# Kernel tuning notes

Measured on AMD Instinct MI355X. Metric: run time of the kernel, lower is better.

Reference implementation:

```python
import jax, jax.numpy as jnp
import numpy as np

G, N, F_IN, D, R, E, L = 512, 128, 64, 128, 4, 1572864, 2  # graphs, nodes/graph, in-feat, embed, relations, edges, gnn layers


def setup_inputs() -> dict:
    key = jax.random.key(0)
    ks = jax.random.split(key, 8)
    x = jax.random.normal(ks[0], (G * N, F_IN), jnp.float32)
    # edges are within-graph (disjoint batched graph, as built by batch_to_gd)
    gid = jax.random.randint(ks[1], (E,), 0, G)
    loc = jax.random.randint(ks[2], (2, E), 0, N)
    edge_index = gid[None, :] * N + loc  # [2, E] (src, dst)
    edge_attr = jax.random.randint(ks[3], (E,), 0, R)
    W_emb = jax.random.normal(ks[4], (F_IN, D), jnp.float32) / np.sqrt(F_IN)
    b_emb = jnp.zeros((D,), jnp.float32)
    W_root = jax.random.normal(ks[5], (L, D, D), jnp.float32) / np.sqrt(D)
    W_rel = jax.random.normal(ks[6], (L, R, D, D), jnp.float32) / np.sqrt(D)
    bias = jnp.zeros((L, D), jnp.float32)
    return {"x": x, "edge_index": edge_index, "edge_attr": edge_attr,
            "W_emb": W_emb, "b_emb": b_emb, "W_root": W_root, "W_rel": W_rel, "bias": bias}


def rgcn_layer(h, edge_index, edge_attr, W_root_l, W_rel_l, bias_l):
    # PyG RGCNConv: out_i = h_i @ W_root + sum_r mean_{j in N_r(i)} (h_j @ W_r) + bias
    n = h.shape[0]
    xr = jnp.einsum('nd,rde->rne', h, W_rel_l)          # [R, n, D] per-relation transform
    src, dst = edge_index[0], edge_index[1]
    msg = xr[edge_attr, src]                             # [E, D] gather per edge
    seg = dst * R + edge_attr                            # combined (node, relation) segment id
    summed = jax.ops.segment_sum(msg, seg, num_segments=n * R)
    cnt = jax.ops.segment_sum(jnp.ones((msg.shape[0],), h.dtype), seg, num_segments=n * R)
    mean = summed / jnp.maximum(cnt, 1.0)[:, None]       # per-relation mean aggregation
    agg = mean.reshape(n, R, -1).sum(axis=1)             # sum over relations
    return h @ W_root_l + agg + bias_l


def reference(x, edge_index, edge_attr, W_emb, b_emb, W_root, W_rel, bias):
    h = x @ W_emb + b_emb                                # embedding_linear
    for l in range(L):                                   # mp_rounds = 1 per layer
        h = jax.nn.relu(rgcn_layer(h, edge_index, edge_attr, W_root[l], W_rel[l], bias[l]))
    # split into per-graph chunks of N nodes and max-pool over nodes
    return jnp.max(h.reshape(G, N, -1), axis=1)          # [G, D]
```

## Files before the change

kernel.cpp:

```cpp
#include <hip/hip_runtime.h>

constexpr int GG    = 512;
constexpr int NPG   = 128;
constexpr int FIN   = 64;
constexpr int DD    = 128;
constexpr int RR    = 4;
constexpr int NN    = GG * NPG;
constexpr int EE    = 1572864;
constexpr int SLC   = 4096;
constexpr int HSTR  = 136;

typedef __attribute__((ext_vector_type(8))) _Float16 f16x8;
typedef __attribute__((ext_vector_type(2))) _Float16 f16x2;
typedef __attribute__((ext_vector_type(4))) float f32x4;
typedef unsigned short u16;
typedef unsigned int   u32;

__device__ __forceinline__ u16 f16b(float x) {
    _Float16 h = (_Float16)x;
    return __builtin_bit_cast(u16, h);
}
__device__ __forceinline__ f16x2 as2(u32 w) { return __builtin_bit_cast(f16x2, w); }

__device__ __forceinline__ void gl_lds16(const void* g, void* l) {
    __builtin_amdgcn_global_load_lds((const __attribute__((address_space(1))) u32*)g,
                                     (__attribute__((address_space(3))) u32*)l, 16, 0, 0);
}


__global__ __launch_bounds__(256, 2) void k_front(const int* __restrict__ ei,
                                                  const int* __restrict__ ea,
                                                  u32* __restrict__ bcur,
                                                  u16* __restrict__ binned,
                                                  const float* __restrict__ W_root,
                                                  const float* __restrict__ W_rel,
                                                  const float* __restrict__ W_emb,
                                                  u16* __restrict__ wtH) {
    __shared__ u32 sRec[4096];
    __shared__ int bh[512];
    __shared__ int lcur[512];
    __shared__ float tile[32 * 129];
    int tid = threadIdx.x;
    int bid = blockIdx.x;

    if (bid < 384) {
        int e0 = bid * 4096;
        bh[tid] = 0; bh[tid + 256] = 0;
        __syncthreads();
        for (int i = 0; i < 16; ++i) {
            int e = e0 + i * 256 + tid;
            int src = ei[e];
            int dst = ei[EE + e];
            int a   = ea[e];
            int g   = dst >> 7;
            u32 rec = (u32)(src & 127) | ((u32)(dst & 127) << 7) | ((u32)a << 14);
            sRec[i * 256 + tid] = rec | ((u32)g << 16);
            atomicAdd(&bh[g], 1);
        }
        __syncthreads();
        lcur[tid]       = tid * SLC +
                          (int)atomicAdd(&bcur[tid], (u32)bh[tid]);
        lcur[tid + 256] = (tid + 256) * SLC +
                          (int)atomicAdd(&bcur[tid + 256], (u32)bh[tid + 256]);
        __syncthreads();
        for (int i = 0; i < 16; ++i) {
            u32 r = sRec[i * 256 + tid];
            int pos = atomicAdd(&lcur[r >> 16], 1);
            binned[pos] = (u16)(r & 0xFFFFu);
        }
    } else if (bid < 424) {
        int pb = bid - 384;
        int mat = pb >> 2;
        int k0 = (pb & 3) * 32;
        int l = mat / 5, m5 = mat - l * 5;
        const float* Wsrc = (m5 == 0) ? (W_root + l * 16384)
                                      : (W_rel + (size_t)(l * RR + (m5 - 1)) * 16384);
        for (int i = 0; i < 16; ++i) {
            int k = k0 + (tid >> 7) + i * 2;
            int n = tid & 127;
            tile[(k - k0) * 129 + n] = Wsrc[k * 128 + n];
        }
        __syncthreads();
        for (int i = 0; i < 16; ++i) {
            int kk = tid & 31;
            int n  = (tid >> 5) + i * 8;
            wtH[mat * 16384 + n * 128 + k0 + kk] = f16b(tile[kk * 129 + n]);
        }
    } else {
        int k0 = (bid - 424) * 32;
        for (int i = 0; i < 16; ++i) {
            int k = k0 + (tid >> 7) + i * 2;
            int n = tid & 127;
            tile[(k - k0) * 129 + n] = W_emb[k * 128 + n];
        }
        __syncthreads();
        for (int i = 0; i < 16; ++i) {
            int kk = tid & 31;
            int n  = (tid >> 5) + i * 8;
            wtH[163840 + n * 64 + k0 + kk] = f16b(tile[kk * 129 + n]);
        }
    }
}


__global__ __launch_bounds__(512, 4) void k_fused(const float* __restrict__ x,
                                                  const float* __restrict__ b_emb,
                                                  float* __restrict__ outF,
                                                  const u16* __restrict__ wtH,
                                                  const float* __restrict__ bias,
                                                  const u16* __restrict__ binned,
                                                  const u32* __restrict__ bcur) {
    __shared__ __align__(16) u16 hG[128 * HSTR];
    __shared__ __align__(16) u16 sQ[2][8192];
    __shared__ __align__(16) u16 sIdx[SLC];
    __shared__ int   sOffs[512];
    __shared__ int   sCnt[512];
    __shared__ float sInv[512];

    int tid  = threadIdx.x;
    int wave = tid >> 6, lane = tid & 63;
    int mm   = lane & 15;
    int qd   = lane >> 4;
    int gr   = blockIdx.x;
    int row0g = gr * NPG;
    int strip = wave * 16;
    const u16* wtE = wtH + 163840;

    auto stage = [&](int step, int bufi) {
        const u16* src = wtH + (step >> 1) * 16384 + (step & 1) * 64;
#pragma unroll
        for (int i = 0; i < 2; ++i) {
            int u = i * 512 + tid;
            int n = u >> 3, j = u & 7;
            gl_lds16(src + n * 128 + ((j ^ (n & 7)) * 8), &sQ[bufi][u * 8]);
        }
    };
    auto stageE = [&](int bufi) {
#pragma unroll
        for (int i = 0; i < 2; ++i) {
            int u = i * 512 + tid;
            int n = u >> 3, j = u & 7;
            gl_lds16(wtE + n * 64 + ((j ^ (n & 7)) * 8), &sQ[bufi][u * 8]);
        }
    };

    f32x4 acc[8];
    auto mfma_half = [&](int bufi, f16x8 A0, f16x8 A1) {
        const u16* buf = sQ[bufi];
#pragma unroll
        for (int nt = 0; nt < 8; ++nt) {
            int n = nt * 16 + mm;
            int g0 = n * 8 + ((0 * 4 + qd) ^ (n & 7));
            int g1 = n * 8 + ((1 * 4 + qd) ^ (n & 7));
            f16x8 B0 = *(const f16x8*)&buf[g0 * 8];
            f16x8 B1 = *(const f16x8*)&buf[g1 * 8];
            f32x4 a = acc[nt];
            a = __builtin_amdgcn_mfma_f32_16x16x32_f16(A0, B0, a, 0, 0, 0);
            a = __builtin_amdgcn_mfma_f32_16x16x32_f16(A1, B1, a, 0, 0, 0);
            acc[nt] = a;
        }
    };

    auto gather = [&](int rel, f16x8* AH) {
        int key = (rel << 7) + strip + mm;
        int r0 = sOffs[key];
        int r1 = sCnt[key];
        _Float16 hs = (_Float16)sInv[key];
        f16x2 sv; sv[0] = hs; sv[1] = hs;
        int cb = qd * 8;
        f16x2 ax[16];
#pragma unroll
        for (int i = 0; i < 16; ++i) ax[i] = (f16x2){(_Float16)0.f, (_Float16)0.f};
        auto add8 = [&](int ks, uint4 u) {
            ax[ks * 4 + 0] += as2(u.x);
            ax[ks * 4 + 1] += as2(u.y);
            ax[ks * 4 + 2] += as2(u.z);
            ax[ks * 4 + 3] += as2(u.w);
        };
        int j = r0;
        for (; j + 2 <= r1; j += 2) {
            int rb0 = (int)sIdx[j]     * HSTR + cb;
            int rb1 = (int)sIdx[j + 1] * HSTR + cb;
            uint4 a0 = *(const uint4*)&hG[rb0];
            uint4 a1 = *(const uint4*)&hG[rb0 + 32];
            uint4 a2 = *(const uint4*)&hG[rb0 + 64];
            uint4 a3 = *(const uint4*)&hG[rb0 + 96];
            uint4 b0 = *(const uint4*)&hG[rb1];
            uint4 b1 = *(const uint4*)&hG[rb1 + 32];
            uint4 b2 = *(const uint4*)&hG[rb1 + 64];
            uint4 b3 = *(const uint4*)&hG[rb1 + 96];
            add8(0, a0); add8(1, a1); add8(2, a2); add8(3, a3);
            add8(0, b0); add8(1, b1); add8(2, b2); add8(3, b3);
        }
        if (j < r1) {
            int rb = (int)sIdx[j] * HSTR + cb;
            uint4 a0 = *(const uint4*)&hG[rb];
            uint4 a1 = *(const uint4*)&hG[rb + 32];
            uint4 a2 = *(const uint4*)&hG[rb + 64];
            uint4 a3 = *(const uint4*)&hG[rb + 96];
            add8(0, a0); add8(1, a1); add8(2, a2); add8(3, a3);
        }
#pragma unroll
        for (int q = 0; q < 4; ++q) {
            union { u32 w[4]; f16x8 v; } o;
#pragma unroll
            for (int t = 0; t < 4; ++t) {
                f16x2 r = ax[q * 4 + t] * sv;
                o.w[t] = __builtin_bit_cast(u32, r);
            }
            AH[q] = o.v;
        }
    };

    stageE(0);
    int cnt = (int)bcur[gr];
    if (cnt > SLC) cnt = SLC;
    uint4 myRec = *(const uint4*)&binned[gr * SLC + tid * 8];
    sCnt[tid] = 0;
    __syncthreads();
    int base8 = tid * 8;
#pragma unroll
    for (int i = 0; i < 8; ++i) {
        if (base8 + i < cnt) {
            u32 w = ((const u32*)&myRec)[i >> 1];
            u32 rec = (i & 1) ? (w >> 16) : (w & 0xFFFFu);
            atomicAdd(&sCnt[rec >> 7], 1);
        }
    }
    __syncthreads();
    int c = sCnt[tid];
    int v = c;
#pragma unroll
    for (int o = 1; o < 64; o <<= 1) {
        int t = __shfl_up(v, o);
        if (lane >= o) v += t;
    }
    int* wtot = (int*)sIdx;
    if (lane == 63) wtot[wave] = v;
    __syncthreads();
    int base = 0;
#pragma unroll
    for (int w = 0; w < 8; ++w) {
        int tw = wtot[w];
        if (w < wave) base += tw;
    }
    int ex = base + v - c;
    sOffs[tid] = ex;
    sCnt[tid]  = ex;
    sInv[tid]  = 1.0f / (float)(c > 0 ? c : 1);
    __syncthreads();
#pragma unroll
    for (int i = 0; i < 8; ++i) {
        if (base8 + i < cnt) {
            u32 w = ((const u32*)&myRec)[i >> 1];
            u32 rec = (i & 1) ? (w >> 16) : (w & 0xFFFFu);
            int pos = atomicAdd(&sCnt[rec >> 7], 1);
            sIdx[pos] = (u16)(rec & 127u);
        }
    }
    __syncthreads();

    {
#pragma unroll
        for (int nt = 0; nt < 8; ++nt) {
            float bv = b_emb[nt * 16 + mm];
            acc[nt] = (f32x4){bv, bv, bv, bv};
        }
        f16x8 AE[2];
#pragma unroll
        for (int ks = 0; ks < 2; ++ks) {
            const float* xp = &x[(size_t)(row0g + strip + mm) * FIN + ks * 32 + qd * 8];
            float4 a = *(const float4*)xp;
            float4 b = *(const float4*)(xp + 4);
            union { u32 w[4]; f16x8 v; } o;
            o.w[0] = (u32)f16b(a.x) | ((u32)f16b(a.y) << 16);
            o.w[1] = (u32)f16b(a.z) | ((u32)f16b(a.w) << 16);
            o.w[2] = (u32)f16b(b.x) | ((u32)f16b(b.y) << 16);
            o.w[3] = (u32)f16b(b.z) | ((u32)f16b(b.w) << 16);
            AE[ks] = o.v;
        }
        stage(0, 1);
        mfma_half(0, AE[0], AE[1]);
#pragma unroll
        for (int nt = 0; nt < 8; ++nt)
#pragma unroll
            for (int r = 0; r < 4; ++r)
                hG[(strip + qd * 4 + r) * HSTR + nt * 16 + mm] =
                    f16b(acc[nt][r]);
        __syncthreads();
    }

    for (int L = 0; L < 2; ++L) {
        const float* bl = bias + L * DD;
#pragma unroll
        for (int i = 0; i < 8; ++i) acc[i] = (f32x4){0.f, 0.f, 0.f, 0.f};

        f16x8 AH[4];
#pragma unroll
        for (int ks = 0; ks < 4; ++ks)
            AH[ks] = *(const f16x8*)&hG[(strip + mm) * HSTR + ks * 32 + qd * 8];

        for (int m = 0; m < 5; ++m) {
#pragma unroll
            for (int h = 0; h < 2; ++h) {
                int s = L * 10 + m * 2 + h;
                if (s + 1 < 20) stage(s + 1, s & 1);
                mfma_half((s + 1) & 1, AH[h * 2], AH[h * 2 + 1]);
                __syncthreads();
            }
            if (m < 4) gather(m, AH);
        }

        if (L == 0) {
#pragma unroll
            for (int nt = 0; nt < 8; ++nt) {
                float bv = bl[nt * 16 + mm];
#pragma unroll
                for (int r = 0; r < 4; ++r)
                    hG[(strip + qd * 4 + r) * HSTR + nt * 16 + mm] =
                        f16b(fmaxf(acc[nt][r] + bv, 0.f));
            }
            __syncthreads();
        } else {
            float* red = (float*)sIdx;
#pragma unroll
            for (int nt = 0; nt < 8; ++nt) {
                float bv = bl[nt * 16 + mm];
                float vv = fmaxf(fmaxf(acc[nt][0], acc[nt][1]),
                                 fmaxf(acc[nt][2], acc[nt][3])) + bv;
                vv = fmaxf(vv, 0.f);
                vv = fmaxf(vv, __shfl_xor(vv, 16));
                vv = fmaxf(vv, __shfl_xor(vv, 32));
                if (lane < 16) red[wave * 128 + nt * 16 + mm] = vv;
            }
            __syncthreads();
            if (tid < 128) {
                float mx = red[tid];
#pragma unroll
                for (int w = 1; w < 8; ++w) mx = fmaxf(mx, red[w * 128 + tid]);
                outF[gr * DD + tid] = mx;
            }
        }
    }
}


extern "C" void kernel_launch(void* const* d_in, const int* in_sizes, int n_in,
                              void* d_out, int out_size, void* d_ws, size_t ws_size,
                              hipStream_t stream) {
    const float* x      = (const float*)d_in[0];
    const int*   ei     = (const int*)  d_in[1];
    const int*   ea     = (const int*)  d_in[2];
    const float* W_emb  = (const float*)d_in[3];
    const float* b_emb  = (const float*)d_in[4];
    const float* W_root = (const float*)d_in[5];
    const float* W_rel  = (const float*)d_in[6];
    const float* bias   = (const float*)d_in[7];
    float* out = (float*)d_out;

    char* p = (char*)d_ws;
    u32* bcur   = (u32*)p; p += 2048;
    u16* binned = (u16*)p; p += (size_t)GG * SLC * 2;
    u16* wtH    = (u16*)p; p += (size_t)(10 * 16384 + 8192) * 2;

    (void)hipMemsetAsync(bcur, 0, 2048, stream);

    k_front<<<426, 256, 0, stream>>>(ei, ea, bcur, binned,
                                     W_root, W_rel, W_emb, wtH);
    k_fused<<<GG, 512, 0, stream>>>(x, b_emb, out, wtH, bias, binned, bcur);
}
```

Before: 164.0 us.

## Locally sort edge records in LDS before binning and pad global bin counters

The binning blocks now do a block-wide prefix scan over per-graph counts, scatter records into a sorted LDS buffer, then write them to global memory in sorted order, so consecutive threads write contiguous runs within each graph's slice instead of scattered 2-byte stores. The global per-graph atomic counters are spread 32 words apart to avoid contention on the same cache line. This adds a scan, extra LDS passes and barriers, and a larger memset.

```diff
diff --git a/kernel.cpp b/kernel.cpp
--- a/kernel.cpp
+++ b/kernel.cpp
@@ -9,6 +9,7 @@
 constexpr int EE    = 1572864;
 constexpr int SLC   = 4096;
 constexpr int HSTR  = 136;
+constexpr int BPAD  = 32;
 
 typedef __attribute__((ext_vector_type(8))) _Float16 f16x8;
 typedef __attribute__((ext_vector_type(2))) _Float16 f16x2;
@@ -39,6 +40,9 @@
     __shared__ u32 sRec[4096];
     __shared__ int bh[512];
     __shared__ int lcur[512];
+    __shared__ int lstart[512];
+    __shared__ int gbase[512];
+    __shared__ int wt4[4];
     __shared__ float tile[32 * 129];
     int tid = threadIdx.x;
     int bid = blockIdx.x;
@@ -58,15 +62,43 @@
             atomicAdd(&bh[g], 1);
         }
         __syncthreads();
-        lcur[tid]       = tid * SLC +
-                          (int)atomicAdd(&bcur[tid], (u32)bh[tid]);
-        lcur[tid + 256] = (tid + 256) * SLC +
-                          (int)atomicAdd(&bcur[tid + 256], (u32)bh[tid + 256]);
-        __syncthreads();
+        int c0 = bh[2 * tid], c1 = bh[2 * tid + 1];
+        int s  = c0 + c1;
+        int v  = s;
+        int lane = tid & 63, wv = tid >> 6;
+#pragma unroll
+        for (int o = 1; o < 64; o <<= 1) {
+            int t = __shfl_up(v, o);
+            if (lane >= o) v += t;
+        }
+        if (lane == 63) wt4[wv] = v;
+        gbase[2 * tid]     = (2 * tid) * SLC +
+                             (int)atomicAdd(&bcur[(2 * tid) * BPAD], (u32)c0);
+        gbase[2 * tid + 1] = (2 * tid + 1) * SLC +
+                             (int)atomicAdd(&bcur[(2 * tid + 1) * BPAD], (u32)c1);
+        __syncthreads();
+        int base = 0;
+#pragma unroll
+        for (int w = 0; w < 4; ++w)
+            if (w < wv) base += wt4[w];
+        int ex = base + v - s;
+        lstart[2 * tid]     = ex;
+        lstart[2 * tid + 1] = ex + c0;
+        lcur[2 * tid]       = ex;
+        lcur[2 * tid + 1]   = ex + c0;
+        __syncthreads();
+        u32* sorted = (u32*)tile;
         for (int i = 0; i < 16; ++i) {
             u32 r = sRec[i * 256 + tid];
             int pos = atomicAdd(&lcur[r >> 16], 1);
-            binned[pos] = (u16)(r & 0xFFFFu);
+            sorted[pos] = r;
+        }
+        __syncthreads();
+        for (int i = 0; i < 16; ++i) {
+            int p = i * 256 + tid;
+            u32 r = sorted[p];
+            int g = r >> 16;
+            binned[gbase[g] + (p - lstart[g])] = (u16)(r & 0xFFFFu);
         }
     } else if (bid < 424) {
         int pb = bid - 384;
@@ -213,7 +245,7 @@
     };
 
     stageE(0);
-    int cnt = (int)bcur[gr];
+    int cnt = (int)bcur[gr * BPAD];
     if (cnt > SLC) cnt = SLC;
     uint4 myRec = *(const uint4*)&binned[gr * SLC + tid * 8];
     sCnt[tid] = 0;
@@ -359,11 +391,11 @@
     float* out = (float*)d_out;
 
     char* p = (char*)d_ws;
-    u32* bcur   = (u32*)p; p += 2048;
+    u32* bcur   = (u32*)p; p += (size_t)512 * BPAD * 4;
     u16* binned = (u16*)p; p += (size_t)GG * SLC * 2;
     u16* wtH    = (u16*)p; p += (size_t)(10 * 16384 + 8192) * 2;
 
-    (void)hipMemsetAsync(bcur, 0, 2048, stream);
+    (void)hipMemsetAsync(bcur, 0, (size_t)512 * BPAD * 4, stream);
 
     k_front<<<426, 256, 0, stream>>>(ei, ea, bcur, binned,
                                      W_root, W_rel, W_emb, wtH);
```

After: 162.2 us. Within noise of the previous version (-1.1%).

## Merge edge binning and weight conversion into fused kernel with grid barrier

Applied to the files above, without the earlier changes.

Folds the separate front kernel (edge binning by graph and weight transpose/fp16 conversion) into the main fused kernel, joined by a software grid-wide barrier on an atomic counter. It removes one kernel launch and its gap. The binning is also reworked: each block sorts its edges locally in LDS and then writes contiguous runs per graph. Per-graph counters are padded to separate cache lines to reduce atomic contention. The cost is that the grid barrier assumes all 512 blocks are co-resident; if they are not, the kernel deadlocks.

```diff
diff --git a/kernel.cpp b/kernel.cpp
--- a/kernel.cpp
+++ b/kernel.cpp
@@ -9,6 +9,8 @@
 constexpr int EE    = 1572864;
 constexpr int SLC   = 4096;
 constexpr int HSTR  = 136;
+constexpr int BPAD  = 32;
+constexpr int WTN   = 10 * 16384 + 8192;
 
 typedef __attribute__((ext_vector_type(8))) _Float16 f16x8;
 typedef __attribute__((ext_vector_type(2))) _Float16 f16x2;
@@ -28,88 +30,19 @@
 }
 
 
-__global__ __launch_bounds__(256, 2) void k_front(const int* __restrict__ ei,
-                                                  const int* __restrict__ ea,
-                                                  u32* __restrict__ bcur,
-                                                  u16* __restrict__ binned,
-                                                  const float* __restrict__ W_root,
-                                                  const float* __restrict__ W_rel,
-                                                  const float* __restrict__ W_emb,
-                                                  u16* __restrict__ wtH) {
-    __shared__ u32 sRec[4096];
-    __shared__ int bh[512];
-    __shared__ int lcur[512];
-    __shared__ float tile[32 * 129];
-    int tid = threadIdx.x;
-    int bid = blockIdx.x;
-
-    if (bid < 384) {
-        int e0 = bid * 4096;
-        bh[tid] = 0; bh[tid + 256] = 0;
-        __syncthreads();
-        for (int i = 0; i < 16; ++i) {
-            int e = e0 + i * 256 + tid;
-            int src = ei[e];
-            int dst = ei[EE + e];
-            int a   = ea[e];
-            int g   = dst >> 7;
-            u32 rec = (u32)(src & 127) | ((u32)(dst & 127) << 7) | ((u32)a << 14);
-            sRec[i * 256 + tid] = rec | ((u32)g << 16);
-            atomicAdd(&bh[g], 1);
-        }
-        __syncthreads();
-        lcur[tid]       = tid * SLC +
-                          (int)atomicAdd(&bcur[tid], (u32)bh[tid]);
-        lcur[tid + 256] = (tid + 256) * SLC +
-                          (int)atomicAdd(&bcur[tid + 256], (u32)bh[tid + 256]);
-        __syncthreads();
-        for (int i = 0; i < 16; ++i) {
-            u32 r = sRec[i * 256 + tid];
-            int pos = atomicAdd(&lcur[r >> 16], 1);
-            binned[pos] = (u16)(r & 0xFFFFu);
-        }
-    } else if (bid < 424) {
-        int pb = bid - 384;
-        int mat = pb >> 2;
-        int k0 = (pb & 3) * 32;
-        int l = mat / 5, m5 = mat - l * 5;
-        const float* Wsrc = (m5 == 0) ? (W_root + l * 16384)
-                                      : (W_rel + (size_t)(l * RR + (m5 - 1)) * 16384);
-        for (int i = 0; i < 16; ++i) {
-            int k = k0 + (tid >> 7) + i * 2;
-            int n = tid & 127;
-            tile[(k - k0) * 129 + n] = Wsrc[k * 128 + n];
-        }
-        __syncthreads();
-        for (int i = 0; i < 16; ++i) {
-            int kk = tid & 31;
-            int n  = (tid >> 5) + i * 8;
-            wtH[mat * 16384 + n * 128 + k0 + kk] = f16b(tile[kk * 129 + n]);
-        }
-    } else {
-        int k0 = (bid - 424) * 32;
-        for (int i = 0; i < 16; ++i) {
-            int k = k0 + (tid >> 7) + i * 2;
-            int n = tid & 127;
-            tile[(k - k0) * 129 + n] = W_emb[k * 128 + n];
-        }
-        __syncthreads();
-        for (int i = 0; i < 16; ++i) {
-            int kk = tid & 31;
-            int n  = (tid >> 5) + i * 8;
-            wtH[163840 + n * 64 + k0 + kk] = f16b(tile[kk * 129 + n]);
-        }
-    }
-}
-
-
 __global__ __launch_bounds__(512, 4) void k_fused(const float* __restrict__ x,
                                                   const float* __restrict__ b_emb,
                                                   float* __restrict__ outF,
-                                                  const u16* __restrict__ wtH,
+                                                  u16* __restrict__ wtH,
                                                   const float* __restrict__ bias,
-                                                  const u16* __restrict__ binned,
-                                                  const u32* __restrict__ bcur) {
+                                                  u16* __restrict__ binned,
+                                                  u32* __restrict__ bcur,
+                                                  u32* __restrict__ gctr,
+                                                  const int* __restrict__ ei,
+                                                  const int* __restrict__ ea,
+                                                  const float* __restrict__ W_root,
+                                                  const float* __restrict__ W_rel,
+                                                  const float* __restrict__ W_emb) {
     __shared__ __align__(16) u16 hG[128 * HSTR];
     __shared__ __align__(16) u16 sQ[2][8192];
     __shared__ __align__(16) u16 sIdx[SLC];
@@ -125,6 +58,90 @@
     int row0g = gr * NPG;
     int strip = wave * 16;
     const u16* wtE = wtH + 163840;
+
+    {
+        int idx = gr * 512 + tid;
+        if (idx < WTN) {
+            float s;
+            if (idx < 163840) {
+                int mat = idx >> 14, rem = idx & 16383;
+                int n = rem >> 7, k = rem & 127;
+                int l = mat / 5, m5 = mat - l * 5;
+                const float* Wsrc = (m5 == 0) ? (W_root + l * 16384)
+                                              : (W_rel + (size_t)(l * RR + (m5 - 1)) * 16384);
+                s = Wsrc[k * 128 + n];
+            } else {
+                int d2 = idx - 163840;
+                int n = d2 >> 6, k = d2 & 63;
+                s = W_emb[k * 128 + n];
+            }
+            wtH[idx] = f16b(s);
+        }
+
+        u32* sRec   = (u32*)&sQ[0][0];
+        u32* sorted = sRec + 3072;
+        int* gbaseA = (int*)(sRec + 6144);
+        int* wt8    = (int*)sIdx;
+        int e0 = gr * 3072;
+        sCnt[tid] = 0;
+        __syncthreads();
+#pragma unroll
+        for (int i = 0; i < 6; ++i) {
+            int e = e0 + i * 512 + tid;
+            int src = ei[e];
+            int dst = ei[EE + e];
+            int a   = ea[e];
+            int g   = dst >> 7;
+            u32 rec = (u32)(src & 127) | ((u32)(dst & 127) << 7) | ((u32)a << 14);
+            sRec[i * 512 + tid] = rec | ((u32)g << 16);
+            atomicAdd(&sCnt[g], 1);
+        }
+        __syncthreads();
+        int c = sCnt[tid], v = c;
+#pragma unroll
+        for (int o = 1; o < 64; o <<= 1) {
+            int t = __shfl_up(v, o);
+            if (lane >= o) v += t;
+        }
+        if (lane == 63) wt8[wave] = v;
+        gbaseA[tid] = tid * SLC +
+                      (int)atomicAdd(&bcur[tid * BPAD], (u32)c);
+        __syncthreads();
+        int bse = 0;
+#pragma unroll
+        for (int w = 0; w < 8; ++w)
+            if (w < wave) bse += wt8[w];
+        int ex = bse + v - c;
+        sOffs[tid] = ex;
+        ((int*)sInv)[tid] = ex;
+        __syncthreads();
+#pragma unroll
+        for (int i = 0; i < 6; ++i) {
+            u32 r = sRec[i * 512 + tid];
+            int pos = atomicAdd(&((int*)sInv)[r >> 16], 1);
+            sorted[pos] = r;
+        }
+        __syncthreads();
+#pragma unroll
+        for (int i = 0; i < 6; ++i) {
+            int p = i * 512 + tid;
+            u32 r = sorted[p];
+            int g = r >> 16;
+            binned[gbaseA[g] + (p - sOffs[g])] = (u16)(r & 0xFFFFu);
+        }
+        __syncthreads();
+    }
+
+    __threadfence();
+    __syncthreads();
+    if (tid == 0) {
+        __hip_atomic_fetch_add(gctr, 1u, __ATOMIC_ACQ_REL, __HIP_MEMORY_SCOPE_AGENT);
+        while (__hip_atomic_load(gctr, __ATOMIC_ACQUIRE, __HIP_MEMORY_SCOPE_AGENT) < (u32)GG)
+            __builtin_amdgcn_s_sleep(8);
+    }
+    __syncthreads();
+    __threadfence();
+
 
     auto stage = [&](int step, int bufi) {
         const u16* src = wtH + (step >> 1) * 16384 + (step & 1) * 64;
@@ -213,7 +230,8 @@
     };
 
     stageE(0);
-    int cnt = (int)bcur[gr];
+    int cnt = (int)__hip_atomic_load(&bcur[gr * BPAD], __ATOMIC_RELAXED,
+                                     __HIP_MEMORY_SCOPE_AGENT);
     if (cnt > SLC) cnt = SLC;
     uint4 myRec = *(const uint4*)&binned[gr * SLC + tid * 8];
     sCnt[tid] = 0;
@@ -359,13 +377,13 @@
     float* out = (float*)d_out;
 
     char* p = (char*)d_ws;
-    u32* bcur   = (u32*)p; p += 2048;
+    u32* bcur   = (u32*)p; p += (size_t)512 * BPAD * 4;
+    u32* gctr   = (u32*)p; p += 128;
     u16* binned = (u16*)p; p += (size_t)GG * SLC * 2;
-    u16* wtH    = (u16*)p; p += (size_t)(10 * 16384 + 8192) * 2;
-
-    (void)hipMemsetAsync(bcur, 0, 2048, stream);
-
-    k_front<<<426, 256, 0, stream>>>(ei, ea, bcur, binned,
-                                     W_root, W_rel, W_emb, wtH);
-    k_fused<<<GG, 512, 0, stream>>>(x, b_emb, out, wtH, bias, binned, bcur);
+    u16* wtH    = (u16*)p; p += (size_t)WTN * 2;
+
+    (void)hipMemsetAsync(bcur, 0, (size_t)512 * BPAD * 4 + 128, stream);
+
+    k_fused<<<GG, 512, 0, stream>>>(x, b_emb, out, wtH, bias, binned, bcur, gctr,
+                                    ei, ea, W_root, W_rel, W_emb);
 }
```

New measurement: 362.6 us. 121% more time.
